# Optimization experiments

Measured on AMD Instinct MI355X. Metric: run time of the kernel, lower is better.

The kernel has to match this reference:

```python
import jax, jax.numpy as jnp
from jax import lax
import numpy as np

S, B, T = 512, 256, 128


def setup_inputs() -> dict:
    key = jax.random.key(0)
    k1, k2, k3, k4 = jax.random.split(key, 4)
    emissions = jax.random.normal(k1, (S, B, T), dtype=jnp.float32)
    mask = jnp.ones((S, B), dtype=jnp.int32)  # all positions valid
    start_transitions = jax.random.normal(k2, (T,), dtype=jnp.float32)
    end_transitions = jax.random.normal(k3, (T,), dtype=jnp.float32)
    transitions = jax.random.normal(k4, (T, T), dtype=jnp.float32)
    return {
        "emissions": emissions,
        "mask": mask,
        "start_transitions": start_transitions,
        "end_transitions": end_transitions,
        "transitions": transitions,
    }


def reference(emissions, mask, start_transitions, end_transitions, transitions):
    """Viterbi decode. emissions: [S,B,T], mask: [S,B].
    Returns (best_tags [B,S] int32, best_path_score [B] float32)."""
    seq_len, batch, num_tags = emissions.shape
    maskb = mask.astype(bool)

    score0 = start_transitions[None, :] + emissions[0]  # [B,T]

    def fwd_step(score, inp):
        em_t, m_t = inp  # [B,T], [B]
        # [B, T_prev, T_next]
        ns = score[:, :, None] + transitions[None, :, :] + em_t[:, None, :]
        next_score = ns.max(axis=1)          # [B,T]
        idx = ns.argmax(axis=1)              # [B,T] best previous tag
        score = jnp.where(m_t[:, None], next_score, score)
        return score, idx

    final_score, history = lax.scan(fwd_step, score0, (emissions[1:], maskb[1:]))
    final_score = final_score + end_transitions[None, :]

    best_last = jnp.argmax(final_score, axis=1)   # [B] tag at last valid position
    best_score = jnp.max(final_score, axis=1)     # [B]

    barange = jnp.arange(batch)

    def back_step(tag, inp):
        hist_t, m_t = inp  # [B,T], [B]
        prev = hist_t[barange, tag]
        tag = jnp.where(m_t, prev, tag)  # only follow history inside the sequence
        return tag, tag

    # reverse scan over transitions t -> t+1 for t = S-2 .. 0; ys[t] = tag at time t
    _, tags_prefix = lax.scan(back_step, best_last, (history, maskb[1:]), reverse=True)
    tags = jnp.concatenate([tags_prefix, best_last[None, :]], axis=0)  # [S,B]
    return tags.T.astype(jnp.int32), best_score
```

## Files before the change

kernel.cpp:

```cpp
#include <hip/hip_runtime.h>

#define SLEN  512
#define BATCH 256
#define NTAGS 128
#define NTHR  512

struct VI { float v; int i; };
__device__ __forceinline__ VI vmax2(VI a, VI b) { return (b.v > a.v) ? b : a; }

__global__ __launch_bounds__(NTHR) void viterbi_kernel(
    const float* __restrict__ em,
    const int*   __restrict__ mask,
    const float* __restrict__ start_t,
    const float* __restrict__ end_t,
    const float* __restrict__ trans,
    float* __restrict__ out)
{
    const int b    = blockIdx.x;
    const int tid  = threadIdx.x;
    const int j    = tid & (NTAGS - 1);
    const int h    = tid >> 7;
    const int base = h << 5;

    __shared__ __align__(16) float sc[NTAGS];
    __shared__ float pmax[4][NTAGS];
    __shared__ int   pidx[4][NTAGS];
    __shared__ int   maskv[SLEN];
    __shared__ unsigned char hist[SLEN - 1][NTAGS];
    __shared__ unsigned char exitc[8][NTAGS];
    __shared__ unsigned char st_tags[8];
    __shared__ unsigned char tagseq[SLEN];
    __shared__ float bestval_s;
    __shared__ int   bestj_s;

    const float* trp = trans + (size_t)base * NTAGS + j;
    const float t00 = trp[ 0*NTAGS], t01 = trp[ 1*NTAGS], t02 = trp[ 2*NTAGS], t03 = trp[ 3*NTAGS];
    const float t04 = trp[ 4*NTAGS], t05 = trp[ 5*NTAGS], t06 = trp[ 6*NTAGS], t07 = trp[ 7*NTAGS];
    const float t08 = trp[ 8*NTAGS], t09 = trp[ 9*NTAGS], t10 = trp[10*NTAGS], t11 = trp[11*NTAGS];
    const float t12 = trp[12*NTAGS], t13 = trp[13*NTAGS], t14 = trp[14*NTAGS], t15 = trp[15*NTAGS];
    const float t16 = trp[16*NTAGS], t17 = trp[17*NTAGS], t18 = trp[18*NTAGS], t19 = trp[19*NTAGS];
    const float t20 = trp[20*NTAGS], t21 = trp[21*NTAGS], t22 = trp[22*NTAGS], t23 = trp[23*NTAGS];
    const float t24 = trp[24*NTAGS], t25 = trp[25*NTAGS], t26 = trp[26*NTAGS], t27 = trp[27*NTAGS];
    const float t28 = trp[28*NTAGS], t29 = trp[29*NTAGS], t30 = trp[30*NTAGS], t31 = trp[31*NTAGS];

    for (int t = tid; t < SLEN; t += NTHR)
        maskv[t] = mask[t * BATCH + b];

    if (tid < NTAGS)
        sc[j] = start_t[j] + em[(size_t)b * NTAGS + j];
    __syncthreads();

    const float* emp = em + (size_t)BATCH * NTAGS + (size_t)b * NTAGS + j;
    float em_next = *emp;

    for (int t = 1; t < SLEN; ++t) {
        const float em_cur = em_next;
        if (t + 1 < SLEN) { emp += BATCH * NTAGS; em_next = *emp; }

        const float4* sq = (const float4*)&sc[base];
        const float4 q0 = sq[0], q1 = sq[1], q2 = sq[2], q3 = sq[3];
        const float4 q4 = sq[4], q5 = sq[5], q6 = sq[6], q7 = sq[7];

        const float c00 = (q0.x + t00) + em_cur, c01 = (q0.y + t01) + em_cur;
        const float c02 = (q0.z + t02) + em_cur, c03 = (q0.w + t03) + em_cur;
        const float c04 = (q1.x + t04) + em_cur, c05 = (q1.y + t05) + em_cur;
        const float c06 = (q1.z + t06) + em_cur, c07 = (q1.w + t07) + em_cur;
        const float c08 = (q2.x + t08) + em_cur, c09 = (q2.y + t09) + em_cur;
        const float c10 = (q2.z + t10) + em_cur, c11 = (q2.w + t11) + em_cur;
        const float c12 = (q3.x + t12) + em_cur, c13 = (q3.y + t13) + em_cur;
        const float c14 = (q3.z + t14) + em_cur, c15 = (q3.w + t15) + em_cur;
        const float c16 = (q4.x + t16) + em_cur, c17 = (q4.y + t17) + em_cur;
        const float c18 = (q4.z + t18) + em_cur, c19 = (q4.w + t19) + em_cur;
        const float c20 = (q5.x + t20) + em_cur, c21 = (q5.y + t21) + em_cur;
        const float c22 = (q5.z + t22) + em_cur, c23 = (q5.w + t23) + em_cur;
        const float c24 = (q6.x + t24) + em_cur, c25 = (q6.y + t25) + em_cur;
        const float c26 = (q6.z + t26) + em_cur, c27 = (q6.w + t27) + em_cur;
        const float c28 = (q7.x + t28) + em_cur, c29 = (q7.y + t29) + em_cur;
        const float c30 = (q7.z + t30) + em_cur, c31 = (q7.w + t31) + em_cur;

        const VI m00 = vmax2(VI{c00, 0}, VI{c01, 1}),  m01 = vmax2(VI{c02, 2}, VI{c03, 3});
        const VI m02 = vmax2(VI{c04, 4}, VI{c05, 5}),  m03 = vmax2(VI{c06, 6}, VI{c07, 7});
        const VI m04 = vmax2(VI{c08, 8}, VI{c09, 9}),  m05 = vmax2(VI{c10,10}, VI{c11,11});
        const VI m06 = vmax2(VI{c12,12}, VI{c13,13}),  m07 = vmax2(VI{c14,14}, VI{c15,15});
        const VI m08 = vmax2(VI{c16,16}, VI{c17,17}),  m09 = vmax2(VI{c18,18}, VI{c19,19});
        const VI m10 = vmax2(VI{c20,20}, VI{c21,21}),  m11 = vmax2(VI{c22,22}, VI{c23,23});
        const VI m12 = vmax2(VI{c24,24}, VI{c25,25}),  m13 = vmax2(VI{c26,26}, VI{c27,27});
        const VI m14 = vmax2(VI{c28,28}, VI{c29,29}),  m15 = vmax2(VI{c30,30}, VI{c31,31});

        const VI n0 = vmax2(m00, m01), n1 = vmax2(m02, m03);
        const VI n2 = vmax2(m04, m05), n3 = vmax2(m06, m07);
        const VI n4 = vmax2(m08, m09), n5 = vmax2(m10, m11);
        const VI n6 = vmax2(m12, m13), n7 = vmax2(m14, m15);

        const VI o0 = vmax2(n0, n1), o1 = vmax2(n2, n3);
        const VI o2 = vmax2(n4, n5), o3 = vmax2(n6, n7);

        const VI p0 = vmax2(o0, o1), p1 = vmax2(o2, o3);
        const VI r  = vmax2(p0, p1);

        pmax[h][j] = r.v;
        pidx[h][j] = base + r.i;
        __syncthreads();

        if (tid < NTAGS) {
            float bv = pmax[0][j]; int bi = pidx[0][j];
            float v1 = pmax[1][j]; int i1 = pidx[1][j];
            if (v1 > bv) { bv = v1; bi = i1; }
            float v2 = pmax[2][j]; int i2 = pidx[2][j];
            if (v2 > bv) { bv = v2; bi = i2; }
            float v3 = pmax[3][j]; int i3 = pidx[3][j];
            if (v3 > bv) { bv = v3; bi = i3; }
            hist[t - 1][j] = (unsigned char)bi;
            if (maskv[t]) sc[j] = bv;
        }
        __syncthreads();
    }

    if (tid < NTAGS) sc[j] = sc[j] + end_t[j];
    __syncthreads();

    if (tid < 64) {
        float v  = sc[tid]; int bj = tid;
        float v1 = sc[tid + 64];
        if (v1 > v) { v = v1; bj = tid + 64; }
#pragma unroll
        for (int off = 32; off > 0; off >>= 1) {
            float ov = __shfl_xor(v, off, 64);
            int   oj = __shfl_xor(bj, off, 64);
            if (ov > v || (ov == v && oj < bj)) { v = ov; bj = oj; }
        }
        if (tid == 0) { bestval_s = v; bestj_s = bj; }
    }
    __syncthreads();

    {
        const int k  = tid & 127;
        const int c0 = tid >> 7;
        const int c1 = c0 + 4;
        int tagA = k, tagB = k;
        for (int u = 63; u >= 0; --u) {
            const int sA = c0 * 64 + u;
            const int sB = c1 * 64 + u;
            if (sB <= SLEN - 2) {
                int pv = hist[sB][tagB];
                tagB = maskv[sB + 1] ? pv : tagB;
            }
            int pv = hist[sA][tagA];
            tagA = maskv[sA + 1] ? pv : tagA;
        }
        exitc[c0][k] = (unsigned char)tagA;
        exitc[c1][k] = (unsigned char)tagB;
    }
    __syncthreads();

    if (tid == 0) {
        int tag = bestj_s;
        for (int c = 7; c >= 0; --c) {
            st_tags[c] = (unsigned char)tag;
            tag = exitc[c][tag];
        }
        out[BATCH * SLEN + b] = bestval_s;
    }
    __syncthreads();

    if (tid < 8) {
        const int c = tid;
        int tag = st_tags[c];
        if (c == 7) tagseq[SLEN - 1] = (unsigned char)tag;
        const int shi = (c == 7) ? (SLEN - 2) : (c * 64 + 63);
        for (int s = shi; s >= c * 64; --s) {
            int pv = hist[s][tag];
            tag = maskv[s + 1] ? pv : tag;
            tagseq[s] = (unsigned char)tag;
        }
    }
    __syncthreads();

    out[b * SLEN + tid] = (float)tagseq[tid];
}

extern "C" void kernel_launch(void* const* d_in, const int* in_sizes, int n_in,
                              void* d_out, int out_size, void* d_ws, size_t ws_size,
                              hipStream_t stream) {
    const float* em      = (const float*)d_in[0];
    const int*   mask    = (const int*)d_in[1];
    const float* start_t = (const float*)d_in[2];
    const float* end_t   = (const float*)d_in[3];
    const float* trans   = (const float*)d_in[4];
    float* out = (float*)d_out;

    viterbi_kernel<<<dim3(BATCH), dim3(NTHR), 0, stream>>>(
        em, mask, start_t, end_t, trans, out);
}
```

Measured before the change: 416.0 us.

## Reduce partial maxima across lanes with DPP and double-buffer scores

Remaps threads so the four partial-max lanes for each tag sit in the same quad, then combines them with DPP quad permutes instead of going through shared memory. The score vector is double-buffered in padded LDS slots, which removes the second __syncthreads per timestep and the serial 128-thread merge phase. This shortens the per-step critical path of the sequential scan. In exchange the em loads are less coalesced, since four lanes read the same element and j varies slowly. The padded layout may also cause LDS bank conflicts on the float4 reads, and launch_bounds now requests 2 blocks per SM.

```diff
diff --git a/kernel.cpp b/kernel.cpp
--- a/kernel.cpp
+++ b/kernel.cpp
@@ -5,10 +5,17 @@
 #define NTAGS 128
 #define NTHR  512
 
+__device__ __forceinline__ int dpp_qperm_b1(int x) {
+    return __builtin_amdgcn_update_dpp(0, x, 0xB1, 0xF, 0xF, true);
+}
+__device__ __forceinline__ int dpp_qperm_4e(int x) {
+    return __builtin_amdgcn_update_dpp(0, x, 0x4E, 0xF, 0xF, true);
+}
+
 struct VI { float v; int i; };
 __device__ __forceinline__ VI vmax2(VI a, VI b) { return (b.v > a.v) ? b : a; }
 
-__global__ __launch_bounds__(NTHR) void viterbi_kernel(
+__global__ __launch_bounds__(NTHR, 2) void viterbi_kernel(
     const float* __restrict__ em,
     const int*   __restrict__ mask,
     const float* __restrict__ start_t,
@@ -18,13 +25,14 @@
 {
     const int b    = blockIdx.x;
     const int tid  = threadIdx.x;
-    const int j    = tid & (NTAGS - 1);
-    const int h    = tid >> 7;
+    const int j    = tid >> 2;
+    const int h    = tid & 3;
     const int base = h << 5;
-
-    __shared__ __align__(16) float sc[NTAGS];
-    __shared__ float pmax[4][NTAGS];
-    __shared__ int   pidx[4][NTAGS];
+    const bool writer = (h == 0);
+    const int jslot = j + (j >> 5) * 8;
+
+    __shared__ __align__(16) float scbuf[2][4 * 40];
+    __shared__ float fin[NTAGS];
     __shared__ int   maskv[SLEN];
     __shared__ unsigned char hist[SLEN - 1][NTAGS];
     __shared__ unsigned char exitc[8][NTAGS];
@@ -46,18 +54,22 @@
     for (int t = tid; t < SLEN; t += NTHR)
         maskv[t] = mask[t * BATCH + b];
 
-    if (tid < NTAGS)
-        sc[j] = start_t[j] + em[(size_t)b * NTAGS + j];
+    float scj = 0.f;
+    if (writer) {
+        scj = start_t[j] + em[(size_t)b * NTAGS + j];
+        scbuf[0][jslot] = scj;
+    }
     __syncthreads();
 
     const float* emp = em + (size_t)BATCH * NTAGS + (size_t)b * NTAGS + j;
     float em_next = *emp;
 
+    int p = 0;
     for (int t = 1; t < SLEN; ++t) {
         const float em_cur = em_next;
         if (t + 1 < SLEN) { emp += BATCH * NTAGS; em_next = *emp; }
 
-        const float4* sq = (const float4*)&sc[base];
+        const float4* sq = (const float4*)&scbuf[p][h * 40];
         const float4 q0 = sq[0], q1 = sq[1], q2 = sq[2], q3 = sq[3];
         const float4 q4 = sq[4], q5 = sq[5], q6 = sq[6], q7 = sq[7];
 
@@ -98,30 +110,34 @@
         const VI p0 = vmax2(o0, o1), p1 = vmax2(o2, o3);
         const VI r  = vmax2(p0, p1);
 
-        pmax[h][j] = r.v;
-        pidx[h][j] = base + r.i;
+        float v  = r.v;
+        int   gi = base + r.i;
+        {
+            float vo = __int_as_float(dpp_qperm_b1(__float_as_int(v)));
+            int   io = dpp_qperm_b1(gi);
+            if (vo > v) { v = vo; gi = io; }
+        }
+        {
+            float vo = __int_as_float(dpp_qperm_4e(__float_as_int(v)));
+            int   io = dpp_qperm_4e(gi);
+            if (vo > v) { v = vo; gi = io; }
+        }
+
+        if (writer) {
+            hist[t - 1][j] = (unsigned char)gi;
+            scj = maskv[t] ? v : scj;
+            scbuf[p ^ 1][jslot] = scj;
+        }
         __syncthreads();
-
-        if (tid < NTAGS) {
-            float bv = pmax[0][j]; int bi = pidx[0][j];
-            float v1 = pmax[1][j]; int i1 = pidx[1][j];
-            if (v1 > bv) { bv = v1; bi = i1; }
-            float v2 = pmax[2][j]; int i2 = pidx[2][j];
-            if (v2 > bv) { bv = v2; bi = i2; }
-            float v3 = pmax[3][j]; int i3 = pidx[3][j];
-            if (v3 > bv) { bv = v3; bi = i3; }
-            hist[t - 1][j] = (unsigned char)bi;
-            if (maskv[t]) sc[j] = bv;
-        }
-        __syncthreads();
-    }
-
-    if (tid < NTAGS) sc[j] = sc[j] + end_t[j];
+        p ^= 1;
+    }
+
+    if (writer) fin[j] = scj + end_t[j];
     __syncthreads();
 
     if (tid < 64) {
-        float v  = sc[tid]; int bj = tid;
-        float v1 = sc[tid + 64];
+        float v  = fin[tid]; int bj = tid;
+        float v1 = fin[tid + 64];
         if (v1 > v) { v = v1; bj = tid + 64; }
 #pragma unroll
         for (int off = 32; off > 0; off >>= 1) {
```

Result: faster. 405.7 us (-2.5%).
